# Kernel optimization log

Measured on AMD Instinct MI355X. Metric: run time of the kernel, lower is better.

Reference implementation:

```python
import jax, jax.numpy as jnp
import numpy as np

F_SIZE = 1000   # feature_size
FIELDS = 39     # field_size
K = 40          # ffm embedding dim
BATCH = 4096
LAYERS = [1024, 512, 256]


def setup_inputs() -> dict:
    key = jax.random.key(0)
    ks = jax.random.split(key, 12)
    inp = {
        "X": jax.random.normal(ks[0], (BATCH, F_SIZE), dtype=jnp.float32),
        "w1": jax.random.normal(ks[1], (F_SIZE,), dtype=jnp.float32) * 0.01,
        "b": jnp.full((1,), 0.5, dtype=jnp.float32),
        "nfk": jax.random.normal(ks[2], (F_SIZE, FIELDS, K), dtype=jnp.float32) * 0.01,
        "f2f": jax.random.randint(ks[3], (F_SIZE,), 0, FIELDS, dtype=jnp.int32),
    }
    dims = [F_SIZE] + LAYERS
    for i in range(len(LAYERS)):
        fan_in, fan_out = dims[i], dims[i + 1]
        scale = np.sqrt(6.0 / (fan_in + fan_out)).astype(np.float32)
        inp[f"deepW{i}"] = jax.random.uniform(ks[4 + i], (fan_in, fan_out), dtype=jnp.float32, minval=-scale, maxval=scale)
        inp[f"deepB{i}"] = jnp.zeros((fan_out,), dtype=jnp.float32)
    scale = np.sqrt(6.0 / (LAYERS[-1] + 1)).astype(np.float32)
    inp["outW"] = jax.random.uniform(ks[10], (LAYERS[-1], 1), dtype=jnp.float32, minval=-scale, maxval=scale)
    inp["outB"] = jnp.zeros((1,), dtype=jnp.float32)
    return inp


def reference(X, w1, b, nfk, f2f, deepW0, deepB0, deepW1, deepB1, deepW2, deepB2, outW, outB):
    # --- linear term: sum_i w1[i]*X[:,i] + b ---
    linear = X @ w1 + b[0]                                  # [B]

    # --- field-aware interaction ---
    # A[i, j, :] = nfk[i, f2f[j], :]  (gather over fields)
    F = nfk.shape[0]
    A = nfk[jnp.arange(F)[:, None], f2f[None, :], :]        # [F, F, K]
    # S[i, j] = <nfk[i, f2f[j]], nfk[j, f2f[i]]> -- batch-independent scalar
    S = jnp.einsum('ijk,jik->ij', A, A)                     # [F, F]
    M = jnp.triu(S, 1)                                      # keep i < j pairs only
    # sum_{i<j} S[i,j] * X[:,i] * X[:,j]
    interaction = jnp.sum((X @ M) * X, axis=1)              # [B]

    # --- deep part (train=False: no dropout) ---
    h = jax.nn.relu(X @ deepW0 + deepB0)
    h = jax.nn.relu(h @ deepW1 + deepB1)
    h = jax.nn.relu(h @ deepW2 + deepB2)
    deep = (h @ outW + outB).reshape(-1)                    # [B]

    out_sum = linear + interaction + deep                   # logits [B]
    return out_sum
```

## Files before the change

### kernel.cpp

```cpp
#include <hip/hip_runtime.h>


#define BATCH   4096
#define FSZ     1000
#define NFIELDS 39
#define KDIM    40

typedef __attribute__((ext_vector_type(8))) short short8v;
typedef __attribute__((ext_vector_type(4))) float f32x4;

__device__ __forceinline__ short f2bf(float f) {
  unsigned u = __builtin_bit_cast(unsigned, f);
  u += 0x7fff + ((u >> 16) & 1);
  return (short)(u >> 16);
}
__device__ __forceinline__ float bf2f(unsigned short h) {
  unsigned u = (unsigned)h << 16;
  return __builtin_bit_cast(float, u);
}

typedef const __attribute__((address_space(1))) unsigned int* gas_ptr;
typedef __attribute__((address_space(3))) unsigned int* las_ptr;
__device__ __forceinline__ void gload16(const void* g, void* l) {
  __builtin_amdgcn_global_load_lds((gas_ptr)g, (las_ptr)l, 16, 0, 0);
}

__global__ __launch_bounds__(256) void prep_nfkT_kernel(
    const float* __restrict__ nfk, unsigned short* __restrict__ nfkT)
{
  int g = blockIdx.x >> 2, jc = blockIdx.x & 3;
  int j = jc * 256 + threadIdx.x;
  if (j < FSZ && g < NFIELDS) {
    const float4* src = (const float4*)(nfk + ((size_t)j * NFIELDS + g) * KDIM);
    short4* dst = (short4*)(nfkT + ((size_t)g * FSZ + j) * KDIM);
    #pragma unroll
    for (int t = 0; t < KDIM / 4; ++t) {
      float4 v = src[t];
      dst[t] = make_short4(f2bf(v.x), f2bf(v.y), f2bf(v.z), f2bf(v.w));
    }
  }
}

__device__ __forceinline__ void transp32(
    const float* __restrict__ in, short* __restrict__ out, int idx, int nx,
    int K_in, int N_in, int Kpad, float (*t)[33], int tid)
{
  int n0 = (idx % nx) * 32, k0 = (idx / nx) * 32;
  int tx = tid & 31, ty = tid >> 5;
  #pragma unroll
  for (int i = 0; i < 32; i += 8) {
    int k = k0 + ty + i, n = n0 + tx;
    t[ty + i][tx] = (k < K_in && n < N_in) ? in[(size_t)k * N_in + n] : 0.f;
  }
  __syncthreads();
  #pragma unroll
  for (int i = 0; i < 32; i += 8) {
    int n = n0 + ty + i, k = k0 + tx;
    if (n < N_in && k < Kpad) out[(size_t)n * Kpad + k] = f2bf(t[tx][ty + i]);
  }
}

__global__ __launch_bounds__(256) void prep_main_kernel(
    const float* __restrict__ X, const float* __restrict__ nfk,
    const unsigned short* __restrict__ nfkT, const int* __restrict__ f2f,
    const float* __restrict__ W0, const float* __restrict__ W1,
    const float* __restrict__ W2,
    short* __restrict__ Xb, short* __restrict__ B12,
    short* __restrict__ Wt1, short* __restrict__ Wt2)
{
  __shared__ float tbuf[32][33];
  __shared__ float C[NFIELDS * 44];
  const int bid = blockIdx.x, tid = threadIdx.x;
  if (bid < 4096) {
    int k = tid * 4;
    short4 o = make_short4(0, 0, 0, 0);
    if (k < FSZ) {
      float4 v = *(const float4*)(X + (size_t)bid * FSZ + k);
      o = make_short4(f2bf(v.x), f2bf(v.y), f2bf(v.z), f2bf(v.w));
    }
    *(short4*)(Xb + (size_t)bid * 1024 + k) = o;
  } else if (bid < 5120) {
    transp32(W0, B12 + 1024 * 1024, bid - 4096, 32, 1000, 1024, 1024, tbuf, tid);
  } else if (bid < 5632) {
    transp32(W1, Wt1, bid - 5120, 16, 1024, 512, 1024, tbuf, tid);
  } else if (bid < 5760) {
    transp32(W2, Wt2, bid - 5632, 8, 512, 256, 512, tbuf, tid);
  } else {
    const int pb = bid - 5760;
    #pragma unroll
    for (int ri = 0; ri < 2; ++ri) {
      const int n = ri ? (1023 - pb) : pb;
      __syncthreads();
      if (n < FSZ) {
        for (int t = tid; t < NFIELDS * KDIM; t += 256)
          C[(t / KDIM) * 44 + (t % KDIM)] = nfk[(size_t)n * (NFIELDS * KDIM) + t];
      }
      __syncthreads();
      int fn = (n < FSZ) ? f2f[n] : 0;
      const unsigned short* pbase = nfkT + (size_t)fn * FSZ * KDIM;
      #pragma unroll
      for (int kk = 0; kk < 4; ++kk) {
        int k = kk * 256 + tid;
        float s = 0.f;
        if (n < FSZ && k < n) {
          int fk = f2f[k];
          const short8v* p = (const short8v*)(pbase + (size_t)k * KDIM);
          const float* q = &C[fk * 44];
          #pragma unroll
          for (int t = 0; t < 5; ++t) {
            short8v v = p[t];
            #pragma unroll
            for (int e = 0; e < 8; ++e)
              s = fmaf(bf2f((unsigned short)v[e]), q[t * 8 + e], s);
          }
        }
        B12[(size_t)n * 1024 + k] = f2bf(s);
      }
    }
  }
}

template<int BM, int BN, int WM, int WN, int EPI>
__global__ __launch_bounds__((BM / WM) * (BN / WN) * 64) void gemm_mfma(
    const short* __restrict__ A, const short* __restrict__ Bt,
    const float* __restrict__ bias, void* __restrict__ Cout,
    int N, int K,
    const short* __restrict__ Xb, const float* __restrict__ w1,
    float* __restrict__ partial,
    const float* __restrict__ c1, const float* __restrict__ c2)
{
  constexpr int WAVES_M = BM / WM, WAVES_N = BN / WN;
  constexpr int NW = WAVES_M * WAVES_N;
  constexpr int AM = WM / 16, AN = WN / 16;
  constexpr int CA = BM / 8;
  constexpr int CB = BN / 8;
  static_assert(CA % NW == 0 && CB % NW == 0, "chunk split");
  __shared__ __align__(16) short As[2][BM * 64];
  __shared__ __align__(16) short Bs[2][BN * 64];
  __shared__ float pbuf[WAVES_N][BM];

  const int nwgx = gridDim.x;
  const int lin  = blockIdx.y * nwgx + blockIdx.x;
  const int cpx  = (nwgx * gridDim.y) >> 3;
  const int slin = (lin & 7) * cpx + (lin >> 3);
  const int bx   = slin % nwgx;
  const int by   = slin / nwgx;

  const int tid  = threadIdx.x;
  const int wid  = tid >> 6;
  const int lane = tid & 63;
  const int wr   = wid / WAVES_N, wc = wid % WAVES_N;
  const int row0 = by * BM;
  const int col0 = bx * BN;

  const int lr8   = lane >> 3;
  const int cbase = (lane & 7) * 16;

  f32x4 acc[AM][AN];
  #pragma unroll
  for (int m = 0; m < AM; ++m)
    #pragma unroll
    for (int n = 0; n < AN; ++n) acc[m][n] = (f32x4)(0.f);

  auto stage = [&](int p, int k0) {
    #pragma unroll
    for (int j = 0; j < CA / NW; ++j) {
      int i = j * NW + wid;
      int r = i * 8 + lr8;
      int cb = cbase ^ ((r & 7) << 4);
      gload16((const char*)A + (((size_t)(row0 + r) * K + k0) << 1) + cb,
              (char*)&As[p][0] + i * 1024);
    }
    #pragma unroll
    for (int j = 0; j < CB / NW; ++j) {
      int i = j * NW + wid;
      int r = i * 8 + lr8;
      int cb = cbase ^ ((r & 7) << 4);
      gload16((const char*)Bt + (((size_t)(col0 + r) * K + k0) << 1) + cb,
              (char*)&Bs[p][0] + i * 1024);
    }
  };

  auto compute = [&](int p) {
    #pragma unroll
    for (int kk = 0; kk < 2; ++kk) {
      const int cb = kk * 64 + (lane >> 4) * 16;
      short8v a[AM], b[AN];
      #pragma unroll
      for (int m = 0; m < AM; ++m) {
        int r = wr * WM + m * 16 + (lane & 15);
        a[m] = *(const short8v*)((const char*)&As[p][0] + r * 128 + (cb ^ ((r & 7) << 4)));
      }
      #pragma unroll
      for (int n = 0; n < AN; ++n) {
        int r = wc * WN + n * 16 + (lane & 15);
        b[n] = *(const short8v*)((const char*)&Bs[p][0] + r * 128 + (cb ^ ((r & 7) << 4)));
      }
      #pragma unroll
      for (int m = 0; m < AM; ++m)
        #pragma unroll
        for (int n = 0; n < AN; ++n)
          acc[m][n] = __builtin_amdgcn_mfma_f32_16x16x32_bf16(a[m], b[n], acc[m][n], 0, 0, 0);
    }
  };

  int nt = K >> 6;
  if (EPI == 0 && bx < 8) {
    int need = bx * 2 + 2;
    nt = nt < need ? nt : need;
  }

  stage(0, 0);
  __syncthreads();
  for (int t = 0; t < nt; ++t) {
    if (t + 1 < nt) stage((t + 1) & 1, (t + 1) << 6);
    compute(t & 1);
    __syncthreads();
  }

  const int cr = (lane >> 4) * 4;
  const int cc = lane & 15;

  if (EPI == 0) {
    if (bx < 8) {
      float rsum[AM * 4];
      #pragma unroll
      for (int i = 0; i < AM * 4; ++i) rsum[i] = 0.f;
      #pragma unroll
      for (int m = 0; m < AM; ++m) {
        #pragma unroll
        for (int n = 0; n < AN; ++n) {
          int gc = col0 + wc * WN + n * 16 + cc;
          float w1v = (gc < FSZ) ? w1[gc] : 0.f;
          #pragma unroll
          for (int r = 0; r < 4; ++r) {
            int gr = row0 + wr * WM + m * 16 + cr + r;
            float xv = bf2f((unsigned short)Xb[(size_t)gr * 1024 + gc]);
            rsum[m * 4 + r] = fmaf(acc[m][n][r] + w1v, xv, rsum[m * 4 + r]);
          }
        }
      }
      #pragma unroll
      for (int mask = 1; mask < 16; mask <<= 1)
        #pragma unroll
        for (int i = 0; i < AM * 4; ++i)
          rsum[i] += __shfl_xor(rsum[i], mask, 64);
      if (cc == 0) {
        #pragma unroll
        for (int m = 0; m < AM; ++m)
          #pragma unroll
          for (int r = 0; r < 4; ++r)
            pbuf[wc][wr * WM + m * 16 + cr + r] = rsum[m * 4 + r];
      }
      __syncthreads();
      if (tid < BM) {
        float s = 0.f;
        #pragma unroll
        for (int w = 0; w < WAVES_N; ++w) s += pbuf[w][tid];
        partial[(size_t)(row0 + tid) * 8 + bx] = s;
      }
    } else {
      #pragma unroll
      for (int m = 0; m < AM; ++m) {
        #pragma unroll
        for (int n = 0; n < AN; ++n) {
          int gc = col0 - 1024 + wc * WN + n * 16 + cc;
          float bv = bias[gc];
          #pragma unroll
          for (int r = 0; r < 4; ++r) {
            int gr = row0 + wr * WM + m * 16 + cr + r;
            float v = fmaxf(acc[m][n][r] + bv, 0.f);
            ((short*)Cout)[(size_t)gr * 1024 + gc] = f2bf(v);
          }
        }
      }
    }
  } else if (EPI == 1) {
    #pragma unroll
    for (int m = 0; m < AM; ++m) {
      #pragma unroll
      for (int n = 0; n < AN; ++n) {
        int gc = col0 + wc * WN + n * 16 + cc;
        float bv = bias[gc];
        #pragma unroll
        for (int r = 0; r < 4; ++r) {
          int gr = row0 + wr * WM + m * 16 + cr + r;
          float v = fmaxf(acc[m][n][r] + bv, 0.f);
          ((short*)Cout)[(size_t)gr * N + gc] = f2bf(v);
        }
      }
    }
  } else {
    float rsum[AM * 4];
    #pragma unroll
    for (int i = 0; i < AM * 4; ++i) rsum[i] = 0.f;
    #pragma unroll
    for (int m = 0; m < AM; ++m) {
      #pragma unroll
      for (int n = 0; n < AN; ++n) {
        int gc = col0 + wc * WN + n * 16 + cc;
        float bv = bias[gc];
        float ow = w1[gc];
        #pragma unroll
        for (int r = 0; r < 4; ++r) {
          float v = fmaxf(acc[m][n][r] + bv, 0.f);
          rsum[m * 4 + r] = fmaf(v, ow, rsum[m * 4 + r]);
        }
      }
    }
    #pragma unroll
    for (int mask = 1; mask < 16; mask <<= 1)
      #pragma unroll
      for (int i = 0; i < AM * 4; ++i)
        rsum[i] += __shfl_xor(rsum[i], mask, 64);
    if (cc == 0) {
      #pragma unroll
      for (int m = 0; m < AM; ++m)
        #pragma unroll
        for (int r = 0; r < 4; ++r)
          pbuf[wc][wr * WM + m * 16 + cr + r] = rsum[m * 4 + r];
    }
    __syncthreads();
    if (tid < BM) {
      int gr = row0 + tid;
      const float4* pp = (const float4*)(partial + (size_t)gr * 8);
      float4 u = pp[0], v = pp[1];
      float s = 0.f;
      #pragma unroll
      for (int w = 0; w < WAVES_N; ++w) s += pbuf[w][tid];
      ((float*)Cout)[gr] = s
          + u.x + u.y + u.z + u.w + v.x + v.y + v.z + v.w + c1[0] + c2[0];
    }
  }
}

extern "C" void kernel_launch(void* const* d_in, const int* in_sizes, int n_in,
                              void* d_out, int out_size, void* d_ws, size_t ws_size,
                              hipStream_t stream) {
  const float* X   = (const float*)d_in[0];
  const float* w1  = (const float*)d_in[1];
  const float* bsc = (const float*)d_in[2];
  const float* nfk = (const float*)d_in[3];
  const int*   f2f = (const int*)d_in[4];
  const float* W0  = (const float*)d_in[5];
  const float* B0  = (const float*)d_in[6];
  const float* W1  = (const float*)d_in[7];
  const float* B1  = (const float*)d_in[8];
  const float* W2  = (const float*)d_in[9];
  const float* B2  = (const float*)d_in[10];
  const float* oW  = (const float*)d_in[11];
  const float* oB  = (const float*)d_in[12];
  float* out = (float*)d_out;

  char* ws = (char*)d_ws;
  short* Xb   = (short*)(ws);
  short* B12  = (short*)(ws + 8388608);
  short* Wt1  = (short*)(ws + 12582912);
  short* Wt2  = (short*)(ws + 13631488);
  float* part = (float*)(ws + 13893632);
  short* h0   = (short*)(ws + 14680064);
  short* h1   = (short*)(ws + 23068672);
  unsigned short* nfkT = (unsigned short*)(ws + 27262976);

  prep_nfkT_kernel<<<156, 256, 0, stream>>>(nfk, nfkT);
  prep_main_kernel<<<6272, 256, 0, stream>>>(X, nfk, nfkT, f2f, W0, W1, W2,
                                             Xb, B12, Wt1, Wt2);
  gemm_mfma<128, 128, 64, 32, 0><<<dim3(16, 32), 512, 0, stream>>>(
      Xb, B12, B0, h0, 2048, 1024, Xb, w1, part, nullptr, nullptr);
  gemm_mfma<64, 64, 16, 32, 1><<<dim3(8, 64), 512, 0, stream>>>(
      h0, Wt1, B1, h1, 512, 1024, nullptr, nullptr, nullptr, nullptr, nullptr);
  gemm_mfma<32, 256, 16, 128, 3><<<dim3(1, 128), 256, 0, stream>>>(
      h1, Wt2, B2, out, 256, 512, nullptr, oW, part, bsc, oB);
}
```

Before: 72.74 us.

## Triple-buffer GEMM LDS staging with prefetch distance two and explicit vmcnt waits

Moves the MFMA GEMM mainloop from double to triple LDS buffering, so global-to-LDS loads run two k-tiles ahead of compute. Each iteration now waits with a partial s_waitcnt vmcnt plus a raw s_barrier instead of a full __syncthreads, so only the tile about to be consumed has to land. The aim is to hide more global load latency behind the MFMAs. In exchange, shared memory per block grows by half, which can lower occupancy, and correctness depends on the vmcnt constant matching the number of loads each thread issues.

```diff
diff --git a/kernel.cpp b/kernel.cpp
--- a/kernel.cpp
+++ b/kernel.cpp
@@ -23,6 +23,14 @@
 typedef __attribute__((address_space(3))) unsigned int* las_ptr;
 __device__ __forceinline__ void gload16(const void* g, void* l) {
   __builtin_amdgcn_global_load_lds((gas_ptr)g, (las_ptr)l, 16, 0, 0);
+}
+
+template<int N> __device__ __forceinline__ void waitcnt_vm() {
+  if constexpr (N == 0)      asm volatile("s_waitcnt vmcnt(0)" ::: "memory");
+  else if constexpr (N == 2) asm volatile("s_waitcnt vmcnt(2)" ::: "memory");
+  else if constexpr (N == 4) asm volatile("s_waitcnt vmcnt(4)" ::: "memory");
+  else if constexpr (N == 9) asm volatile("s_waitcnt vmcnt(9)" ::: "memory");
+  else static_assert(N == 0 || N == 2 || N == 4 || N == 9, "add vmcnt case");
 }
 
 __global__ __launch_bounds__(256) void prep_nfkT_kernel(
@@ -134,9 +142,10 @@
   constexpr int AM = WM / 16, AN = WN / 16;
   constexpr int CA = BM / 8;
   constexpr int CB = BN / 8;
+  constexpr int L  = CA / NW + CB / NW;
   static_assert(CA % NW == 0 && CB % NW == 0, "chunk split");
-  __shared__ __align__(16) short As[2][BM * 64];
-  __shared__ __align__(16) short Bs[2][BN * 64];
+  __shared__ __align__(16) short As[3][BM * 64];
+  __shared__ __align__(16) short Bs[3][BN * 64];
   __shared__ float pbuf[WAVES_N][BM];
 
   const int nwgx = gridDim.x;
@@ -211,11 +220,26 @@
   }
 
   stage(0, 0);
-  __syncthreads();
+  if (nt > 1) {
+    stage(1, 64);
+    waitcnt_vm<L>();
+  } else {
+    waitcnt_vm<0>();
+  }
+  __builtin_amdgcn_s_barrier();
+  __builtin_amdgcn_sched_barrier(0);
+  int p = 0, pw = 2;
   for (int t = 0; t < nt; ++t) {
-    if (t + 1 < nt) stage((t + 1) & 1, (t + 1) << 6);
-    compute(t & 1);
-    __syncthreads();
+    if (t + 2 < nt) stage(pw, (t + 2) << 6);
+    compute(p);
+    if (t + 1 < nt) {
+      if (t + 2 < nt) waitcnt_vm<L>();
+      else            waitcnt_vm<0>();
+      __builtin_amdgcn_s_barrier();
+      __builtin_amdgcn_sched_barrier(0);
+    }
+    p  = (p == 2) ? 0 : p + 1;
+    pw = (pw == 2) ? 0 : pw + 1;
   }
 
   const int cr = (lane >> 4) * 4;
```

New measurement: 87.20 us. 1.2x slower.
